# Kernel tuning notes

Hardware: AMD Instinct MI355X
Metric: run time of the kernel (lower is better)

The kernel has to match this reference:

```python
import jax, jax.numpy as jnp
import numpy as np
from jax import lax

INFLAT = 10.0  # fixed-point inflation constant (module-level global in original repo)


def _qconv(x, shift, mag, stride, pad):
    # Conv2dInt8: sum((input << shift) * mag) == conv with weight 2**shift * mag
    w = jnp.exp2(shift.astype(jnp.float32)) * mag.astype(jnp.float32)  # (O,I,kh,kw)
    return lax.conv_general_dilated(
        x, w, window_strides=(stride, stride),
        padding=[(pad, pad), (pad, pad)],
        dimension_numbers=('NCHW', 'OIHW', 'NCHW'))


def _bn_q(y, alpha, beta, q):
    # BN with zero bias_power: round((alpha*conv + beta*2^(Q+INFLAT)) * 2^-INFLAT), clamp int8
    off = beta * jnp.exp2(q.astype(jnp.float32) + INFLAT)  # per out-channel
    out = jnp.round((alpha[None, :, None, None] * y + off[None, :, None, None])
                    * jnp.float32(2.0 ** (-INFLAT)))
    return jnp.clip(out, -128.0, 127.0)


def setup_inputs() -> dict:
    key = jax.random.key(0)
    ks = jax.random.split(key, 16)
    N, C_in, H, W = 32, 256, 56, 56
    width, C_out = 64, 256
    x = jax.random.randint(ks[0], (N, C_in, H, W), -128, 128).astype(jnp.float32)
    # conv1: 1x1 256->64 ; conv2: 3x3 64->64 ; conv3: 1x1 64->256
    s1 = jax.random.randint(ks[1], (width, C_in, 1, 1), 0, 4)
    m1 = jax.random.randint(ks[2], (width, C_in, 1, 1), -3, 4)
    a1 = jax.random.uniform(ks[3], (width,), minval=0.0005, maxval=0.002)
    b1 = jax.random.normal(ks[4], (width,))
    q1 = jax.random.randint(ks[5], (width,), 0, 3)
    s2 = jax.random.randint(ks[6], (width, width, 3, 3), 0, 4)
    m2 = jax.random.randint(ks[7], (width, width, 3, 3), -3, 4)
    a2 = jax.random.uniform(ks[8], (width,), minval=0.0005, maxval=0.002)
    b2 = jax.random.normal(ks[9], (width,))
    q2 = jax.random.randint(ks[10], (width,), 0, 3)
    s3 = jax.random.randint(ks[11], (C_out, width, 1, 1), 0, 4)
    m3 = jax.random.randint(ks[12], (C_out, width, 1, 1), -3, 4)
    a3 = jax.random.uniform(ks[13], (C_out,), minval=0.0005, maxval=0.002)
    b3 = jax.random.normal(ks[14], (C_out,))
    q3 = jax.random.randint(ks[15], (C_out,), 0, 3)
    return dict(x=x, s1=s1, m1=m1, a1=a1, b1=b1, q1=q1,
                s2=s2, m2=m2, a2=a2, b2=b2, q2=q2,
                s3=s3, m3=m3, a3=a3, b3=b3, q3=q3)


def reference(x, s1, m1, a1, b1, q1, s2, m2, a2, b2, q2, s3, m3, a3, b3, q3):
    identity = x  # int8-valued
    # conv1 (1x1, stride 1, pad 0) + BN + clamp + relu
    out = _qconv(x, s1, m1, stride=1, pad=0)
    out = jax.nn.relu(_bn_q(out, a1, b1, q1))
    # conv2 (3x3, stride=self.stride=1, pad 1) + BN + clamp + relu
    out = _qconv(out, s2, m2, stride=1, pad=1)
    out = jax.nn.relu(_bn_q(out, a2, b2, q2))
    # conv3 (1x1, stride 1, pad 0) + BN + clamp
    out = _qconv(out, s3, m3, stride=1, pad=0)
    out = _bn_q(out, a3, b3, q3)
    # residual add (int16 in original), clamp to int8, relu
    out = jnp.clip(out + identity, -128.0, 127.0)
    return jax.nn.relu(out)
```

## Files before the change

kernel.cpp:

```cpp
#include <hip/hip_runtime.h>
#include <stdint.h>

#define HW 3136
#define IMGW 56
#define NIMG 32

typedef int i32x4 __attribute__((ext_vector_type(4)));

static __device__ __forceinline__ float bnq(float alpha, float off, int acc) {
  float t = __fmul_rn(alpha, (float)acc);
  t = __fadd_rn(t, off);
  t = __fmul_rn(t, 0x1p-10f);
  float r = rintf(t);
  return fminf(fmaxf(r, -128.0f), 127.0f);
}

__global__ void prep_kernel(
    const int* __restrict__ s1, const int* __restrict__ m1,
    const float* __restrict__ a1, const float* __restrict__ b1, const int* __restrict__ q1,
    const int* __restrict__ s2, const int* __restrict__ m2,
    const float* __restrict__ a2, const float* __restrict__ b2, const int* __restrict__ q2,
    const int* __restrict__ s3, const int* __restrict__ m3,
    const float* __restrict__ a3, const float* __restrict__ b3, const int* __restrict__ q3,
    int* __restrict__ w1m, int* __restrict__ w2m, int* __restrict__ w3m,
    float* __restrict__ a1p, float* __restrict__ o1p,
    float* __restrict__ a2p, float* __restrict__ o2p,
    float* __restrict__ a3p, float* __restrict__ o3p)
{
  int t = blockIdx.x * blockDim.x + threadIdx.x;
  int nthr = gridDim.x * blockDim.x;

  for (int i = t; i < 4096; i += nthr) {
    int jw = i & 3, l = (i >> 2) & 63;
    int rest = i >> 8;
    int s = rest & 3, kk = rest >> 2;
    int c = l & 15, g = l >> 4;
    int co = s * 16 + c;
    int p = 0;
    for (int b = 0; b < 4; ++b) {
      int ci = kk * 64 + g * 16 + jw * 4 + b;
      int idx = co * 256 + ci;
      int w = m1[idx] * (1 << s1[idx]);
      p |= (w & 0xFF) << (8 * b);
    }
    w1m[i] = p;
  }
  for (int i = t; i < 9216; i += nthr) {
    int jw = i & 3, l = (i >> 2) & 63;
    int rest = i >> 8;
    int s = rest & 3, tap = rest >> 2;
    int c = l & 15, g = l >> 4;
    int co = s * 16 + c;
    int ky = tap / 3, kx = tap - ky * 3;
    int p = 0;
    for (int b = 0; b < 4; ++b) {
      int ci = g * 16 + jw * 4 + b;
      int idx = ((co * 64 + ci) * 3 + ky) * 3 + kx;
      int w = m2[idx] * (1 << s2[idx]);
      p |= (w & 0xFF) << (8 * b);
    }
    w2m[i] = p;
  }
  for (int i = t; i < 4096; i += nthr) {
    int jw = i & 3, l = (i >> 2) & 63;
    int rest = i >> 8;
    int nt = rest & 3, s = rest >> 2;
    int c = l & 15, g = l >> 4;
    int co = s * 64 + nt * 16 + c;
    int p = 0;
    for (int b = 0; b < 4; ++b) {
      int ci = g * 16 + jw * 4 + b;
      int idx = co * 64 + ci;
      int w = m3[idx] * (1 << s3[idx]);
      p |= (w & 0xFF) << (8 * b);
    }
    w3m[i] = p;
  }
  for (int i = t; i < 64; i += nthr) {
    a1p[i] = a1[i];
    o1p[i] = __fmul_rn(b1[i], exp2f((float)q1[i] + 10.0f));
    a2p[i] = a2[i];
    o2p[i] = __fmul_rn(b2[i], exp2f((float)q2[i] + 10.0f));
  }
  for (int i = t; i < 256; i += nthr) {
    a3p[i] = a3[i];
    o3p[i] = __fmul_rn(b3[i], exp2f((float)q3[i] + 10.0f));
  }
}

__global__ __launch_bounds__(256) void k01_pack_conv1(
    const float* __restrict__ x,
    const int* __restrict__ w1m,
    const float* __restrict__ a1p, const float* __restrict__ o1p,
    int* __restrict__ x8p, int* __restrict__ y1p)
{
  __shared__ int ldsx[64 * 68];

  int tid = threadIdx.x;

  {
    int o = tid & 3;
    int p = tid >> 2;
    size_t pg = (size_t)blockIdx.x * 64 + p;
    int n = (int)(pg / HW);
    int pos = (int)(pg - (size_t)n * HW);
    const float* xb = x + ((size_t)n * 256 + o * 64) * HW + pos;

    float f[64];
#pragma unroll
    for (int k = 0; k < 64; ++k) f[k] = xb[(size_t)k * HW];
    __builtin_amdgcn_sched_barrier(0);

    int4 ov[4];
#pragma unroll
    for (int g = 0; g < 4; ++g) {
      int wds[4];
#pragma unroll
      for (int wdi = 0; wdi < 4; ++wdi) {
        int c0 = g * 16 + wdi * 4;
        wds[wdi] = ((int)f[c0] & 0xFF) | (((int)f[c0 + 1] & 0xFF) << 8) |
                   (((int)f[c0 + 2] & 0xFF) << 16) | (((int)f[c0 + 3] & 0xFF) << 24);
      }
      ov[g].x = wds[0]; ov[g].y = wds[1]; ov[g].z = wds[2]; ov[g].w = wds[3];
    }

    int* gb = x8p + pg * 64 + o * 16;
#pragma unroll
    for (int g = 0; g < 4; ++g) ((int4*)gb)[g] = ov[g];
    int* lb = &ldsx[p * 68 + o * 16];
#pragma unroll
    for (int g = 0; g < 4; ++g) *(int4*)(lb + g * 4) = ov[g];
  }
  __syncthreads();

  int lane = tid & 63;
  int sW = __builtin_amdgcn_readfirstlane(tid >> 6);
  int c = lane & 15, g = lane >> 4;

  i32x4 acc[4];
#pragma unroll
  for (int mt = 0; mt < 4; ++mt) acc[mt] = (i32x4){0, 0, 0, 0};

#pragma unroll
  for (int kk = 0; kk < 4; ++kk) {
    i32x4 bf = *(const i32x4*)(w1m + ((kk * 4 + sW) * 64 + lane) * 4);
#pragma unroll
    for (int mt = 0; mt < 4; ++mt) {
      i32x4 af = *(const i32x4*)(ldsx + (mt * 16 + c) * 68 + kk * 16 + g * 4);
      acc[mt] = __builtin_amdgcn_mfma_i32_16x16x64_i8(af, bf, acc[mt], 0, 0, 0);
    }
  }

  float al = a1p[sW * 16 + c], of = o1p[sW * 16 + c];
  char* yb = (char*)y1p;
  size_t pb = (size_t)blockIdx.x * 64;
#pragma unroll
  for (int mt = 0; mt < 4; ++mt) {
#pragma unroll
    for (int r = 0; r < 4; ++r) {
      float rv = bnq(al, of, acc[mt][r]);
      int v = (int)rv;
      if (v < 0) v = 0;
      yb[(pb + mt * 16 + g * 4 + r) * 64 + sW * 16 + c] = (char)v;
    }
  }
}

__global__ __launch_bounds__(256) void k23_conv23(
    const int* __restrict__ y1p,
    const int* __restrict__ w2m,
    const float* __restrict__ a2p, const float* __restrict__ o2p,
    const int* __restrict__ w3m,
    const float* __restrict__ a3p, const float* __restrict__ o3p,
    const int* __restrict__ x8p,
    float* __restrict__ out)
{
  __shared__ __align__(16) char smem[25600];
  int4* halo = (int4*)smem;
  char* ldsyB = smem + 20480;

  int t0 = (blockIdx.x & 7) * 196 + (blockIdx.x >> 3);
  int n = t0 / 49;
  int bl = t0 - n * 49;
  int p0l = bl * 64;

  int tid = threadIdx.x;
  int lane = tid & 63;
  int sW = __builtin_amdgcn_readfirstlane(tid >> 6);
  int h0 = p0l / IMGW;

  const int4* src = (const int4*)y1p;
#pragma unroll
  for (int i = 0; i < 4; ++i) {
    int idx = tid + i * 256;
    if (idx < 928) {
      int pp = idx >> 2, chunk = idx & 3;
      int r = pp / 58, col = pp - r * 58;
      int hh = h0 - 1 + r;
      int4 v = make_int4(0, 0, 0, 0);
      if ((unsigned)hh < 56u && col >= 1 && col <= 56)
        v = src[((size_t)n * HW + (size_t)hh * IMGW + (col - 1)) * 4 + chunk];
      halo[pp * 5 + chunk] = v;
    }
  }

  size_t pg = (size_t)n * HW + p0l + lane;
  const i32x4* ra = (const i32x4*)(x8p + pg * 64 + sW * 16);
  i32x4 rq0 = ra[0], rq1 = ra[1], rq2 = ra[2], rq3 = ra[3];

  __syncthreads();

  int c = lane & 15, g = lane >> 4;

  int cen[4];
#pragma unroll
  for (int mt = 0; mt < 4; ++mt) {
    int pos = p0l + mt * 16 + c;
    int hh = pos / IMGW, ww = pos - hh * IMGW;
    cen[mt] = (hh - h0 + 1) * 58 + ww + 1;
  }

  i32x4 acc[4];
#pragma unroll
  for (int mt = 0; mt < 4; ++mt) acc[mt] = (i32x4){0, 0, 0, 0};

#pragma unroll
  for (int tap = 0; tap < 9; ++tap) {
    i32x4 bf = *(const i32x4*)(w2m + ((tap * 4 + sW) * 64 + lane) * 4);
    int ky = tap / 3, kx = tap - ky * 3;
    int d = (ky - 1) * 58 + (kx - 1);
#pragma unroll
    for (int mt = 0; mt < 4; ++mt) {
      i32x4 af = *(const i32x4*)&halo[(cen[mt] + d) * 5 + g];
      acc[mt] = __builtin_amdgcn_mfma_i32_16x16x64_i8(af, bf, acc[mt], 0, 0, 0);
    }
  }

  {
    float al = a2p[sW * 16 + c], of = o2p[sW * 16 + c];
#pragma unroll
    for (int mt = 0; mt < 4; ++mt) {
#pragma unroll
      for (int r = 0; r < 4; ++r) {
        float rv = bnq(al, of, acc[mt][r]);
        int v = (int)rv;
        if (v < 0) v = 0;
        ldsyB[(mt * 16 + g * 4 + r) * 80 + sW * 16 + c] = (char)v;
      }
    }
  }
  __syncthreads();

  int* Dw = (int*)smem + sW * 1280;
  int posl = p0l + lane;
  float* ob = out + (size_t)n * 256 * HW + posl;

#pragma unroll
  for (int nt = 0; nt < 4; ++nt) {
    i32x4 bf = *(const i32x4*)(w3m + ((sW * 4 + nt) * 64 + lane) * 4);
#pragma unroll
    for (int mt = 0; mt < 4; ++mt) {
      i32x4 af = *(const i32x4*)(ldsyB + (mt * 16 + c) * 80 + g * 16);
      i32x4 z = {0, 0, 0, 0};
      i32x4 D = __builtin_amdgcn_mfma_i32_16x16x64_i8(af, bf, z, 0, 0, 0);
      Dw[(mt * 16 + g * 4 + 0) * 20 + c] = D[0];
      Dw[(mt * 16 + g * 4 + 1) * 20 + c] = D[1];
      Dw[(mt * 16 + g * 4 + 2) * 20 + c] = D[2];
      Dw[(mt * 16 + g * 4 + 3) * 20 + c] = D[3];
    }
    i32x4 q0 = *(const i32x4*)(Dw + lane * 20 + 0);
    i32x4 q1 = *(const i32x4*)(Dw + lane * 20 + 4);
    i32x4 q2 = *(const i32x4*)(Dw + lane * 20 + 8);
    i32x4 q3 = *(const i32x4*)(Dw + lane * 20 + 12);
    i32x4 rqn = nt == 0 ? rq0 : (nt == 1 ? rq1 : (nt == 2 ? rq2 : rq3));
#pragma unroll
    for (int cc = 0; cc < 16; ++cc) {
      int accv = cc < 4 ? q0[cc] : cc < 8 ? q1[cc - 4] : cc < 12 ? q2[cc - 8] : q3[cc - 12];
      int co = sW * 64 + nt * 16 + cc;
      float rv = bnq(a3p[co], o3p[co], accv);
      int ip = rqn[cc >> 2];
      int id = (int)(int8_t)(ip >> (8 * (cc & 3)));
      int v = (int)rv + id;
      v = v > 127 ? 127 : v;
      v = v < 0 ? 0 : v;
      ob[(size_t)co * HW] = (float)v;
    }
  }
}

extern "C" void kernel_launch(void* const* d_in, const int* in_sizes, int n_in,
                              void* d_out, int out_size, void* d_ws, size_t ws_size,
                              hipStream_t stream) {
  const float* x  = (const float*)d_in[0];
  const int*   s1 = (const int*)d_in[1];
  const int*   m1 = (const int*)d_in[2];
  const float* a1 = (const float*)d_in[3];
  const float* b1 = (const float*)d_in[4];
  const int*   q1 = (const int*)d_in[5];
  const int*   s2 = (const int*)d_in[6];
  const int*   m2 = (const int*)d_in[7];
  const float* a2 = (const float*)d_in[8];
  const float* b2 = (const float*)d_in[9];
  const int*   q2 = (const int*)d_in[10];
  const int*   s3 = (const int*)d_in[11];
  const int*   m3 = (const int*)d_in[12];
  const float* a3 = (const float*)d_in[13];
  const float* b3 = (const float*)d_in[14];
  const int*   q3 = (const int*)d_in[15];

  char* ws = (char*)d_ws;
  int* w1m = (int*)(ws + 0);
  int* w2m = (int*)(ws + 16384);
  int* w3m = (int*)(ws + 53248);
  float* a1p = (float*)(ws + 69632);
  float* o1p = (float*)(ws + 69888);
  float* a2p = (float*)(ws + 70144);
  float* o2p = (float*)(ws + 70400);
  float* a3p = (float*)(ws + 70656);
  float* o3p = (float*)(ws + 71680);
  int* y1p = (int*)(ws + 73728);
  int* x8p = (int*)(ws + 73728 + 6422528);

  prep_kernel<<<64, 256, 0, stream>>>(s1, m1, a1, b1, q1,
                                      s2, m2, a2, b2, q2,
                                      s3, m3, a3, b3, q3,
                                      w1m, w2m, w3m,
                                      a1p, o1p, a2p, o2p, a3p, o3p);

  k01_pack_conv1<<<(NIMG * HW) / 64, 256, 0, stream>>>(x, w1m, a1p, o1p, x8p, y1p);
  k23_conv23<<<(NIMG * HW) / 64, 256, 0, stream>>>(y1p, w2m, a2p, o2p,
                                                   w3m, a3p, o3p, x8p,
                                                   (float*)d_out);
}
```

Baseline: 64.57 us.

## Fuse conv1 into conv2/conv3 kernel with halo recompute, drop intermediate buffers

Merges the pack+conv1 kernel into the conv2/conv3 kernel. Each block loads the float input for its 64-pixel tile plus a 3-row halo (232 pixels), packs it to int8 in LDS and computes conv1 over the whole halo. The residual is then read from LDS, so the int8 copy of x and the y1 intermediate no longer go through global memory. The price is about 3.6x redundant conv1 compute and input reads per tile, 53KB of LDS per block, which lowers occupancy, and 60 accumulator registers.

```diff
diff --git a/kernel.cpp b/kernel.cpp
--- a/kernel.cpp
+++ b/kernel.cpp
@@ -88,141 +88,119 @@
   }
 }
 
-__global__ __launch_bounds__(256) void k01_pack_conv1(
+__global__ __launch_bounds__(256) void kfused(
     const float* __restrict__ x,
-    const int* __restrict__ w1m,
-    const float* __restrict__ a1p, const float* __restrict__ o1p,
-    int* __restrict__ x8p, int* __restrict__ y1p)
+    const int* __restrict__ w1m, const float* __restrict__ a1p, const float* __restrict__ o1p,
+    const int* __restrict__ w2m, const float* __restrict__ a2p, const float* __restrict__ o2p,
+    const int* __restrict__ w3m, const float* __restrict__ a3p, const float* __restrict__ o3p,
+    float* __restrict__ out)
 {
-  __shared__ int ldsx[64 * 68];
+  __shared__ __align__(16) char smem[53120];
+  int*  xt  = (int*)smem;
+  char* y1t = smem + 34560;
+  char* y2t = smem;
+
+  int t0 = (blockIdx.x & 7) * 196 + (blockIdx.x >> 3);
+  int n = t0 / 49, bl = t0 - n * 49;
+  int p0l = bl * 64;
+  int h0 = p0l / IMGW;
 
   int tid = threadIdx.x;
-
-  {
-    int o = tid & 3;
-    int p = tid >> 2;
-    size_t pg = (size_t)blockIdx.x * 64 + p;
-    int n = (int)(pg / HW);
-    int pos = (int)(pg - (size_t)n * HW);
-    const float* xb = x + ((size_t)n * 256 + o * 64) * HW + pos;
-
-    float f[64];
-#pragma unroll
-    for (int k = 0; k < 64; ++k) f[k] = xb[(size_t)k * HW];
-    __builtin_amdgcn_sched_barrier(0);
-
-    int4 ov[4];
-#pragma unroll
-    for (int g = 0; g < 4; ++g) {
-      int wds[4];
-#pragma unroll
-      for (int wdi = 0; wdi < 4; ++wdi) {
-        int c0 = g * 16 + wdi * 4;
-        wds[wdi] = ((int)f[c0] & 0xFF) | (((int)f[c0 + 1] & 0xFF) << 8) |
-                   (((int)f[c0 + 2] & 0xFF) << 16) | (((int)f[c0 + 3] & 0xFF) << 24);
-      }
-      ov[g].x = wds[0]; ov[g].y = wds[1]; ov[g].z = wds[2]; ov[g].w = wds[3];
-    }
-
-    int* gb = x8p + pg * 64 + o * 16;
-#pragma unroll
-    for (int g = 0; g < 4; ++g) ((int4*)gb)[g] = ov[g];
-    int* lb = &ldsx[p * 68 + o * 16];
-#pragma unroll
-    for (int g = 0; g < 4; ++g) *(int4*)(lb + g * 4) = ov[g];
-  }
-  __syncthreads();
-
   int lane = tid & 63;
   int sW = __builtin_amdgcn_readfirstlane(tid >> 6);
   int c = lane & 15, g = lane >> 4;
 
-  i32x4 acc[4];
-#pragma unroll
-  for (int mt = 0; mt < 4; ++mt) acc[mt] = (i32x4){0, 0, 0, 0};
-
-#pragma unroll
-  for (int kk = 0; kk < 4; ++kk) {
-    i32x4 bf = *(const i32x4*)(w1m + ((kk * 4 + sW) * 64 + lane) * 4);
-#pragma unroll
-    for (int mt = 0; mt < 4; ++mt) {
-      i32x4 af = *(const i32x4*)(ldsx + (mt * 16 + c) * 68 + kk * 16 + g * 4);
-      acc[mt] = __builtin_amdgcn_mfma_i32_16x16x64_i8(af, bf, acc[mt], 0, 0, 0);
-    }
-  }
-
-  float al = a1p[sW * 16 + c], of = o1p[sW * 16 + c];
-  char* yb = (char*)y1p;
-  size_t pb = (size_t)blockIdx.x * 64;
-#pragma unroll
-  for (int mt = 0; mt < 4; ++mt) {
-#pragma unroll
-    for (int r = 0; r < 4; ++r) {
-      float rv = bnq(al, of, acc[mt][r]);
-      int v = (int)rv;
-      if (v < 0) v = 0;
-      yb[(pb + mt * 16 + g * 4 + r) * 64 + sW * 16 + c] = (char)v;
-    }
-  }
-}
-
-__global__ __launch_bounds__(256) void k23_conv23(
-    const int* __restrict__ y1p,
-    const int* __restrict__ w2m,
-    const float* __restrict__ a2p, const float* __restrict__ o2p,
-    const int* __restrict__ w3m,
-    const float* __restrict__ a3p, const float* __restrict__ o3p,
-    const int* __restrict__ x8p,
-    float* __restrict__ out)
-{
-  __shared__ __align__(16) char smem[25600];
-  int4* halo = (int4*)smem;
-  char* ldsyB = smem + 20480;
-
-  int t0 = (blockIdx.x & 7) * 196 + (blockIdx.x >> 3);
-  int n = t0 / 49;
-  int bl = t0 - n * 49;
-  int p0l = bl * 64;
-
-  int tid = threadIdx.x;
-  int lane = tid & 63;
-  int sW = __builtin_amdgcn_readfirstlane(tid >> 6);
-  int h0 = p0l / IMGW;
-
-  const int4* src = (const int4*)y1p;
-#pragma unroll
-  for (int i = 0; i < 4; ++i) {
-    int idx = tid + i * 256;
-    if (idx < 928) {
-      int pp = idx >> 2, chunk = idx & 3;
-      int r = pp / 58, col = pp - r * 58;
-      int hh = h0 - 1 + r;
-      int4 v = make_int4(0, 0, 0, 0);
-      if ((unsigned)hh < 56u && col >= 1 && col <= 56)
-        v = src[((size_t)n * HW + (size_t)hh * IMGW + (col - 1)) * 4 + chunk];
-      halo[pp * 5 + chunk] = v;
-    }
-  }
-
-  size_t pg = (size_t)n * HW + p0l + lane;
-  const i32x4* ra = (const i32x4*)(x8p + pg * 64 + sW * 16);
-  i32x4 rq0 = ra[0], rq1 = ra[1], rq2 = ra[2], rq3 = ra[3];
-
+  int pp = tid;
+  int r58 = pp / 58, col = pp - r58 * 58;
+  int phh = h0 - 1 + r58, pww = col - 1;
+  bool pvalid = (pp < 232) && ((unsigned)phh < 56u) && ((unsigned)pww < 56u);
+  const float* xb = x + (size_t)n * 256 * HW + phh * IMGW + pww;
+
+  int P = p0l + lane;
+  int hP = P / IMGW, wP = P - hP * IMGW;
+  int ppc = (hP - h0 + 1) * 58 + wP + 1;
+
+  i32x4 acc1[15];
+#pragma unroll
+  for (int i = 0; i < 15; ++i) acc1[i] = (i32x4){0, 0, 0, 0};
+  i32x4 rq0 = (i32x4){0,0,0,0}, rq1 = rq0, rq2 = rq0, rq3 = rq0;
+
+#pragma unroll
+  for (int hf = 0; hf < 2; ++hf) {
+    if (pvalid) {
+#pragma unroll
+      for (int bb = 0; bb < 2; ++bb) {
+        float f[64];
+#pragma unroll
+        for (int k = 0; k < 64; ++k)
+          f[k] = xb[(size_t)(hf * 128 + bb * 64 + k) * HW];
+        __builtin_amdgcn_sched_barrier(0);
+#pragma unroll
+        for (int w = 0; w < 16; ++w) {
+          int wd = ((int)f[w * 4] & 0xFF) | (((int)f[w * 4 + 1] & 0xFF) << 8) |
+                   (((int)f[w * 4 + 2] & 0xFF) << 16) | (((int)f[w * 4 + 3] & 0xFF) << 24);
+          xt[pp * 36 + bb * 16 + w] = wd;
+        }
+      }
+    } else if (pp < 240) {
+#pragma unroll
+      for (int w = 0; w < 32; ++w) xt[pp * 36 + w] = 0;
+    }
+    __syncthreads();
+
+    if ((sW >> 1) == hf) {
+      int bw = (sW & 1) * 16;
+      rq0 = *(const i32x4*)(xt + ppc * 36 + bw + 0);
+      rq1 = *(const i32x4*)(xt + ppc * 36 + bw + 4);
+      rq2 = *(const i32x4*)(xt + ppc * 36 + bw + 8);
+      rq3 = *(const i32x4*)(xt + ppc * 36 + bw + 12);
+    }
+
+#pragma unroll
+    for (int kk = 0; kk < 2; ++kk) {
+      int kkg = hf * 2 + kk;
+      i32x4 bf = *(const i32x4*)(w1m + ((kkg * 4 + sW) * 64 + lane) * 4);
+#pragma unroll
+      for (int mt = 0; mt < 15; ++mt) {
+        i32x4 af = *(const i32x4*)(xt + (mt * 16 + c) * 36 + kk * 16 + g * 4);
+        acc1[mt] = __builtin_amdgcn_mfma_i32_16x16x64_i8(af, bf, acc1[mt], 0, 0, 0);
+      }
+    }
+    __syncthreads();
+  }
+
+  {
+    float al = a1p[sW * 16 + c], of = o1p[sW * 16 + c];
+#pragma unroll
+    for (int mt = 0; mt < 15; ++mt) {
+#pragma unroll
+      for (int r = 0; r < 4; ++r) {
+        int prow = mt * 16 + g * 4 + r;
+        if (prow < 232) {
+          int pr = prow / 58, pc = prow - pr * 58;
+          int ph = h0 - 1 + pr;
+          bool pv = ((unsigned)ph < 56u) && (pc >= 1) && (pc <= 56);
+          float rv = bnq(al, of, acc1[mt][r]);
+          int v = (int)rv;
+          if (v < 0) v = 0;
+          y1t[prow * 80 + sW * 16 + c] = pv ? (char)v : (char)0;
+        }
+      }
+    }
+  }
   __syncthreads();
-
-  int c = lane & 15, g = lane >> 4;
 
   int cen[4];
 #pragma unroll
   for (int mt = 0; mt < 4; ++mt) {
     int pos = p0l + mt * 16 + c;
-    int hh = pos / IMGW, ww = pos - hh * IMGW;
-    cen[mt] = (hh - h0 + 1) * 58 + ww + 1;
-  }
-
-  i32x4 acc[4];
-#pragma unroll
-  for (int mt = 0; mt < 4; ++mt) acc[mt] = (i32x4){0, 0, 0, 0};
+    int hh2 = pos / IMGW, ww2 = pos - hh2 * IMGW;
+    cen[mt] = (hh2 - h0 + 1) * 58 + ww2 + 1;
+  }
+
+  i32x4 acc2[4];
+#pragma unroll
+  for (int i = 0; i < 4; ++i) acc2[i] = (i32x4){0, 0, 0, 0};
 
 #pragma unroll
   for (int tap = 0; tap < 9; ++tap) {
@@ -231,8 +209,8 @@
     int d = (ky - 1) * 58 + (kx - 1);
 #pragma unroll
     for (int mt = 0; mt < 4; ++mt) {
-      i32x4 af = *(const i32x4*)&halo[(cen[mt] + d) * 5 + g];
-      acc[mt] = __builtin_amdgcn_mfma_i32_16x16x64_i8(af, bf, acc[mt], 0, 0, 0);
+      i32x4 af = *(const i32x4*)(y1t + (cen[mt] + d) * 80 + g * 16);
+      acc2[mt] = __builtin_amdgcn_mfma_i32_16x16x64_i8(af, bf, acc2[mt], 0, 0, 0);
     }
   }
 
@@ -242,16 +220,16 @@
     for (int mt = 0; mt < 4; ++mt) {
 #pragma unroll
       for (int r = 0; r < 4; ++r) {
-        float rv = bnq(al, of, acc[mt][r]);
+        float rv = bnq(al, of, acc2[mt][r]);
         int v = (int)rv;
         if (v < 0) v = 0;
-        ldsyB[(mt * 16 + g * 4 + r) * 80 + sW * 16 + c] = (char)v;
+        y2t[(mt * 16 + g * 4 + r) * 80 + sW * 16 + c] = (char)v;
       }
     }
   }
   __syncthreads();
 
-  int* Dw = (int*)smem + sW * 1280;
+  int* Dw = (int*)(smem + 5120) + sW * 1280;
   int posl = p0l + lane;
   float* ob = out + (size_t)n * 256 * HW + posl;
 
@@ -260,7 +238,7 @@
     i32x4 bf = *(const i32x4*)(w3m + ((sW * 4 + nt) * 64 + lane) * 4);
 #pragma unroll
     for (int mt = 0; mt < 4; ++mt) {
-      i32x4 af = *(const i32x4*)(ldsyB + (mt * 16 + c) * 80 + g * 16);
+      i32x4 af = *(const i32x4*)(y2t + (mt * 16 + c) * 80 + g * 16);
       i32x4 z = {0, 0, 0, 0};
       i32x4 D = __builtin_amdgcn_mfma_i32_16x16x64_i8(af, bf, z, 0, 0, 0);
       Dw[(mt * 16 + g * 4 + 0) * 20 + c] = D[0];
@@ -318,8 +296,6 @@
   float* o2p = (float*)(ws + 70400);
   float* a3p = (float*)(ws + 70656);
   float* o3p = (float*)(ws + 71680);
-  int* y1p = (int*)(ws + 73728);
-  int* x8p = (int*)(ws + 73728 + 6422528);
 
   prep_kernel<<<64, 256, 0, stream>>>(s1, m1, a1, b1, q1,
                                       s2, m2, a2, b2, q2,
@@ -327,8 +303,6 @@
                                       w1m, w2m, w3m,
                                       a1p, o1p, a2p, o2p, a3p, o3p);
 
-  k01_pack_conv1<<<(NIMG * HW) / 64, 256, 0, stream>>>(x, w1m, a1p, o1p, x8p, y1p);
-  k23_conv23<<<(NIMG * HW) / 64, 256, 0, stream>>>(y1p, w2m, a2p, o2p,
-                                                   w3m, a3p, o3p, x8p,
-                                                   (float*)d_out);
+  kfused<<<(NIMG * HW) / 64, 256, 0, stream>>>(
+      x, w1m, a1p, o1p, w2m, a2p, o2p, w3m, a3p, o3p, (float*)d_out);
 }
```

After: 77.55 us. +20.1%, slower.

## Process 128 pixels per block in fused conv2/conv3 kernel to amortize halo loads

Applied to the files above, without the earlier changes.

The conv2+conv3 kernel now handles 128 output pixels per block instead of 64, with a larger halo tile (6 rows) in shared memory and 8 MFMA row tiles per wave for the 3x3 conv. This reduces redundant halo reloads and per-block weight loads, and cuts the grid from 1568 to 800 blocks, with the last block per image handling only 64 pixels. It costs more registers and LDS, plus an extra barrier because the conv2 output buffer now reuses the halo region, which may lower occupancy.

```diff
diff --git a/kernel.cpp b/kernel.cpp
--- a/kernel.cpp
+++ b/kernel.cpp
@@ -175,25 +175,26 @@
     const int* __restrict__ x8p,
     float* __restrict__ out)
 {
-  __shared__ __align__(16) char smem[25600];
+  __shared__ __align__(16) char smem[30720];
   int4* halo = (int4*)smem;
-  char* ldsyB = smem + 20480;
-
-  int t0 = (blockIdx.x & 7) * 196 + (blockIdx.x >> 3);
-  int n = t0 / 49;
-  int bl = t0 - n * 49;
-  int p0l = bl * 64;
+  char* y2t  = smem;
+
+  int t0 = (blockIdx.x & 7) * 100 + (blockIdx.x >> 3);
+  int n = t0 / 25, bl = t0 - n * 25;
+  int p0l = bl * 128;
+  int validB = (bl < 24);
+  int h0 = p0l / IMGW;
 
   int tid = threadIdx.x;
   int lane = tid & 63;
   int sW = __builtin_amdgcn_readfirstlane(tid >> 6);
-  int h0 = p0l / IMGW;
+  int c = lane & 15, g = lane >> 4;
 
   const int4* src = (const int4*)y1p;
 #pragma unroll
-  for (int i = 0; i < 4; ++i) {
+  for (int i = 0; i < 6; ++i) {
     int idx = tid + i * 256;
-    if (idx < 928) {
+    if (idx < 1392) {
       int pp = idx >> 2, chunk = idx & 3;
       int r = pp / 58, col = pp - r * 58;
       int hh = h0 - 1 + r;
@@ -204,25 +205,26 @@
     }
   }
 
-  size_t pg = (size_t)n * HW + p0l + lane;
-  const i32x4* ra = (const i32x4*)(x8p + pg * 64 + sW * 16);
-  i32x4 rq0 = ra[0], rq1 = ra[1], rq2 = ra[2], rq3 = ra[3];
+  size_t pgA = (size_t)n * HW + p0l + lane;
+  size_t pgB = validB ? (pgA + 64) : pgA;
+  const i32x4* ra = (const i32x4*)(x8p + pgA * 64 + sW * 16);
+  const i32x4* rb = (const i32x4*)(x8p + pgB * 64 + sW * 16);
+  i32x4 rqA0 = ra[0], rqA1 = ra[1], rqA2 = ra[2], rqA3 = ra[3];
+  i32x4 rqB0 = rb[0], rqB1 = rb[1], rqB2 = rb[2], rqB3 = rb[3];
 
   __syncthreads();
 
-  int c = lane & 15, g = lane >> 4;
-
-  int cen[4];
-#pragma unroll
-  for (int mt = 0; mt < 4; ++mt) {
+  int cen[8];
+#pragma unroll
+  for (int mt = 0; mt < 8; ++mt) {
     int pos = p0l + mt * 16 + c;
-    int hh = pos / IMGW, ww = pos - hh * IMGW;
-    cen[mt] = (hh - h0 + 1) * 58 + ww + 1;
-  }
-
-  i32x4 acc[4];
-#pragma unroll
-  for (int mt = 0; mt < 4; ++mt) acc[mt] = (i32x4){0, 0, 0, 0};
+    int hh2 = pos / IMGW, ww2 = pos - hh2 * IMGW;
+    cen[mt] = (hh2 - h0 + 1) * 58 + ww2 + 1;
+  }
+
+  i32x4 acc2[8];
+#pragma unroll
+  for (int i = 0; i < 8; ++i) acc2[i] = (i32x4){0, 0, 0, 0};
 
 #pragma unroll
   for (int tap = 0; tap < 9; ++tap) {
@@ -230,60 +232,66 @@
     int ky = tap / 3, kx = tap - ky * 3;
     int d = (ky - 1) * 58 + (kx - 1);
 #pragma unroll
-    for (int mt = 0; mt < 4; ++mt) {
+    for (int mt = 0; mt < 8; ++mt) {
       i32x4 af = *(const i32x4*)&halo[(cen[mt] + d) * 5 + g];
-      acc[mt] = __builtin_amdgcn_mfma_i32_16x16x64_i8(af, bf, acc[mt], 0, 0, 0);
-    }
-  }
+      acc2[mt] = __builtin_amdgcn_mfma_i32_16x16x64_i8(af, bf, acc2[mt], 0, 0, 0);
+    }
+  }
+  __syncthreads();
 
   {
     float al = a2p[sW * 16 + c], of = o2p[sW * 16 + c];
 #pragma unroll
-    for (int mt = 0; mt < 4; ++mt) {
+    for (int mt = 0; mt < 8; ++mt) {
 #pragma unroll
       for (int r = 0; r < 4; ++r) {
-        float rv = bnq(al, of, acc[mt][r]);
+        float rv = bnq(al, of, acc2[mt][r]);
         int v = (int)rv;
         if (v < 0) v = 0;
-        ldsyB[(mt * 16 + g * 4 + r) * 80 + sW * 16 + c] = (char)v;
+        y2t[(mt * 16 + g * 4 + r) * 80 + sW * 16 + c] = (char)v;
       }
     }
   }
   __syncthreads();
 
-  int* Dw = (int*)smem + sW * 1280;
-  int posl = p0l + lane;
-  float* ob = out + (size_t)n * 256 * HW + posl;
-
-#pragma unroll
-  for (int nt = 0; nt < 4; ++nt) {
-    i32x4 bf = *(const i32x4*)(w3m + ((sW * 4 + nt) * 64 + lane) * 4);
-#pragma unroll
-    for (int mt = 0; mt < 4; ++mt) {
-      i32x4 af = *(const i32x4*)(ldsyB + (mt * 16 + c) * 80 + g * 16);
-      i32x4 z = {0, 0, 0, 0};
-      i32x4 D = __builtin_amdgcn_mfma_i32_16x16x64_i8(af, bf, z, 0, 0, 0);
-      Dw[(mt * 16 + g * 4 + 0) * 20 + c] = D[0];
-      Dw[(mt * 16 + g * 4 + 1) * 20 + c] = D[1];
-      Dw[(mt * 16 + g * 4 + 2) * 20 + c] = D[2];
-      Dw[(mt * 16 + g * 4 + 3) * 20 + c] = D[3];
-    }
-    i32x4 q0 = *(const i32x4*)(Dw + lane * 20 + 0);
-    i32x4 q1 = *(const i32x4*)(Dw + lane * 20 + 4);
-    i32x4 q2 = *(const i32x4*)(Dw + lane * 20 + 8);
-    i32x4 q3 = *(const i32x4*)(Dw + lane * 20 + 12);
-    i32x4 rqn = nt == 0 ? rq0 : (nt == 1 ? rq1 : (nt == 2 ? rq2 : rq3));
-#pragma unroll
-    for (int cc = 0; cc < 16; ++cc) {
-      int accv = cc < 4 ? q0[cc] : cc < 8 ? q1[cc - 4] : cc < 12 ? q2[cc - 8] : q3[cc - 12];
-      int co = sW * 64 + nt * 16 + cc;
-      float rv = bnq(a3p[co], o3p[co], accv);
-      int ip = rqn[cc >> 2];
-      int id = (int)(int8_t)(ip >> (8 * (cc & 3)));
-      int v = (int)rv + id;
-      v = v > 127 ? 127 : v;
-      v = v < 0 ? 0 : v;
-      ob[(size_t)co * HW] = (float)v;
+  int* Dw = (int*)(smem + 10240) + sW * 1280;
+
+#pragma unroll
+  for (int ph = 0; ph < 2; ++ph) {
+    if (ph == 1 && !validB) break;
+    float* ob = out + (size_t)n * 256 * HW + p0l + ph * 64 + lane;
+#pragma unroll
+    for (int nt = 0; nt < 4; ++nt) {
+      i32x4 bf = *(const i32x4*)(w3m + ((sW * 4 + nt) * 64 + lane) * 4);
+#pragma unroll
+      for (int mtl = 0; mtl < 4; ++mtl) {
+        i32x4 af = *(const i32x4*)(y2t + ((ph * 4 + mtl) * 16 + c) * 80 + g * 16);
+        i32x4 z = {0, 0, 0, 0};
+        i32x4 D = __builtin_amdgcn_mfma_i32_16x16x64_i8(af, bf, z, 0, 0, 0);
+        Dw[(mtl * 16 + g * 4 + 0) * 20 + c] = D[0];
+        Dw[(mtl * 16 + g * 4 + 1) * 20 + c] = D[1];
+        Dw[(mtl * 16 + g * 4 + 2) * 20 + c] = D[2];
+        Dw[(mtl * 16 + g * 4 + 3) * 20 + c] = D[3];
+      }
+      i32x4 q0 = *(const i32x4*)(Dw + lane * 20 + 0);
+      i32x4 q1 = *(const i32x4*)(Dw + lane * 20 + 4);
+      i32x4 q2 = *(const i32x4*)(Dw + lane * 20 + 8);
+      i32x4 q3 = *(const i32x4*)(Dw + lane * 20 + 12);
+      i32x4 rqn;
+      if (ph == 0) rqn = nt == 0 ? rqA0 : (nt == 1 ? rqA1 : (nt == 2 ? rqA2 : rqA3));
+      else         rqn = nt == 0 ? rqB0 : (nt == 1 ? rqB1 : (nt == 2 ? rqB2 : rqB3));
+#pragma unroll
+      for (int cc = 0; cc < 16; ++cc) {
+        int accv = cc < 4 ? q0[cc] : cc < 8 ? q1[cc - 4] : cc < 12 ? q2[cc - 8] : q3[cc - 12];
+        int co = sW * 64 + nt * 16 + cc;
+        float rv = bnq(a3p[co], o3p[co], accv);
+        int ip = rqn[cc >> 2];
+        int id = (int)(int8_t)(ip >> (8 * (cc & 3)));
+        int v = (int)rv + id;
+        v = v > 127 ? 127 : v;
+        v = v < 0 ? 0 : v;
+        ob[(size_t)co * HW] = (float)v;
+      }
     }
   }
 }
@@ -328,7 +336,7 @@
                                       a1p, o1p, a2p, o2p, a3p, o3p);
 
   k01_pack_conv1<<<(NIMG * HW) / 64, 256, 0, stream>>>(x, w1m, a1p, o1p, x8p, y1p);
-  k23_conv23<<<(NIMG * HW) / 64, 256, 0, stream>>>(y1p, w2m, a2p, o2p,
-                                                   w3m, a3p, o3p, x8p,
-                                                   (float*)d_out);
-}
+  k23_conv23<<<800, 256, 0, stream>>>(y1p, w2m, a2p, o2p,
+                                      w3m, a3p, o3p, x8p,
+                                      (float*)d_out);
+}
```

New measurement: 69.61 us. 7.8% more time.
